# Optimization experiments

Hardware: AMD Instinct MI355X
Metric: run time of the kernel (lower is better)

## Reference

```python
import jax, jax.numpy as jnp
import numpy as np

D = 896      # mm_hidden_size
H = 8        # num heads
HD = D // H  # head dim = 112
M = 8        # num_memory_tokens
P = 196      # patch_size
EPS = 1e-12


def _layernorm(x, g, b):
    mu = jnp.mean(x, axis=-1, keepdims=True)
    var = jnp.mean(jnp.square(x - mu), axis=-1, keepdims=True)
    return (x - mu) * jax.lax.rsqrt(var + EPS) * g + b


def setup_inputs() -> dict:
    key = jax.random.key(0)
    ks = jax.random.split(key, 12)
    F = 32
    s = 0.02
    return {
        "image_features": jax.random.normal(ks[0], (F, P, D), jnp.float32),
        "initial_memory": jax.random.normal(ks[1], (M, P, D), jnp.float32),
        "qW": jax.random.normal(ks[2], (D, D), jnp.float32) * s,
        "qb": jnp.zeros((D,), jnp.float32),
        "kW": jax.random.normal(ks[3], (D, D), jnp.float32) * s,
        "kb": jnp.zeros((D,), jnp.float32),
        "vW": jax.random.normal(ks[4], (D, D), jnp.float32) * s,
        "vb": jnp.zeros((D,), jnp.float32),
        "oW": jax.random.normal(ks[5], (D, D), jnp.float32) * s,
        "ob": jnp.zeros((D,), jnp.float32),
        "ln1_g": jnp.ones((D,), jnp.float32),
        "ln1_b": jnp.zeros((D,), jnp.float32),
        "mW": jax.random.normal(ks[6], (D, 4 * D), jnp.float32) * s,
        "mb": jnp.zeros((4 * D,), jnp.float32),
        "pW": jax.random.normal(ks[7], (4 * D, D), jnp.float32) * s,
        "pb": jnp.zeros((D,), jnp.float32),
        "ln2_g": jnp.ones((D,), jnp.float32),
        "ln2_b": jnp.zeros((D,), jnp.float32),
    }


def reference(image_features, initial_memory, qW, qb, kW, kb, vW, vb,
              oW, ob, ln1_g, ln1_b, mW, mb, pW, pb, ln2_g, ln2_b):
    F = image_features.shape[0]
    Lq = M * P            # 1568 query tokens
    Lk = F * P            # kv tokens
    mem = initial_memory.reshape(1, Lq, D)      # [1, Lq, D]
    img = image_features.reshape(1, Lk, D)      # [1, Lk, D]

    def heads(x, L):
        return x.reshape(1, L, H, HD).transpose(0, 2, 1, 3)  # [1,H,L,hd]

    q = heads(mem @ qW + qb, Lq)
    k = heads(img @ kW + kb, Lk)
    v = heads(img @ vW + vb, Lk)

    scores = jnp.einsum('bhqd,bhkd->bhqk', q, k) / np.sqrt(HD).astype(jnp.float32)
    probs = jax.nn.softmax(scores, axis=-1)                  # [1,H,Lq,Lk]
    ctx = jnp.einsum('bhqk,bhkd->bhqd', probs, v)
    ctx = ctx.transpose(0, 2, 1, 3).reshape(1, Lq, D)

    # residual + layernorm epilogue of Attention
    attn_out = _layernorm(ctx @ oW + ob + mem, ln1_g, ln1_b)

    # MLP -> residual + layernorm
    hidden = jax.nn.relu(attn_out @ mW + mb)                 # [1, Lq, 4D]
    out = _layernorm(hidden @ pW + pb + attn_out, ln2_g, ln2_b)

    # frame attention scores: sum over heads and query tokens, avg per frame
    attn_sum = probs.sum(axis=(1, 2))[0]                     # [Lk]
    frame_scores = attn_sum.reshape(F, P).mean(axis=1)       # [F]

    final_memory = out.reshape(M, P, D)
    return final_memory, frame_scores
```

## Files before the change

kernel.cpp:

```cpp
#include <hip/hip_runtime.h>
#include <hip/hip_bf16.h>
#include <math.h>

#define TP_D   896
#define TP_H   8
#define TP_HD  112
#define TP_LQ  1568
#define TP_LK  6272
#define TP_D4  3584
#define TP_F   32
#define TP_P   196

typedef unsigned short u16;
typedef float f32x4 __attribute__((ext_vector_type(4)));
typedef __bf16 bf16x8 __attribute__((ext_vector_type(8)));

__device__ inline float bf2f(u16 u) {
    return __uint_as_float(((unsigned int)u) << 16);
}
__device__ inline u16 f2bf(float f) {
    unsigned int x = __float_as_uint(f);
    unsigned int lsb = (x >> 16) & 1u;
    x += 0x7fffu + lsb;
    return (u16)(x >> 16);
}
__device__ inline ushort4 pack4(float a, float b, float c, float d) {
    return make_ushort4(f2bf(a), f2bf(b), f2bf(c), f2bf(d));
}
__device__ inline int pidx(int row, int col) {
    return row * 128 + (col ^ ((row & 7) << 3));
}

__global__ void cast_f32_bf16(const float* __restrict__ src, u16* __restrict__ dst, int n) {
    int i = (blockIdx.x * blockDim.x + threadIdx.x) * 4;
    if (i + 3 < n) {
        float4 v = *(const float4*)(src + i);
        *(ushort4*)(dst + i) = pack4(v.x, v.y, v.z, v.w);
    } else {
        for (; i < n; ++i) dst[i] = f2bf(src[i]);
    }
}

__global__ void cast_div_bf16(const float* __restrict__ src, const float* __restrict__ l,
                              u16* __restrict__ dst) {
    int i = (blockIdx.x * 256 + threadIdx.x) * 4;
    if (i >= TP_LQ * TP_D) return;
    int q = i / TP_D;
    int col = i - q * TP_D;
    int h = col / TP_HD;
    float inv = 1.f / l[h * TP_LQ + q];
    float4 v = *(const float4*)(src + i);
    *(ushort4*)(dst + i) = pack4(v.x * inv, v.y * inv, v.z * inv, v.w * inv);
}

__global__ void transpose_cast(const float* __restrict__ src, u16* __restrict__ dst, int R, int C) {
    __shared__ float t[32][33];
    int bx = blockIdx.x * 32;
    int by = blockIdx.y * 32;
    int tx = threadIdx.x, ty = threadIdx.y;
#pragma unroll
    for (int j = 0; j < 4; ++j)
        t[ty + j * 8][tx] = src[(size_t)(by + ty + j * 8) * C + bx + tx];
    __syncthreads();
#pragma unroll
    for (int j = 0; j < 4; ++j)
        dst[(size_t)(bx + ty + j * 8) * R + by + tx] = f2bf(t[tx][ty + j * 8]);
}

struct GemmParams {
    const u16* A;  long long aZ; int lda;
    const u16* Bt; long long bZ; int ldb;
    int M, N, K;
    const float* bias;
    float* outF;
    u16* outB; long long cZ; int ldc;
    float scale;
    int hbase;
    int relu;
    int kc;
};

#define LDS_STRIDE 56

template <int MODE>
__global__ __launch_bounds__(256, 2) void gemm_bf16(GemmParams p) {
    __shared__ u16 lsA[128 * LDS_STRIDE];
    __shared__ u16 lsB[128 * LDS_STRIDE];

    const int tid = threadIdx.x;
    const int z = blockIdx.z;
    const u16* A;
    const u16* Bt;
    if (MODE == 6) {
        A  = p.A  + (size_t)z * p.kc;
        Bt = p.Bt + (size_t)z * p.kc;
    } else {
        A  = p.A  + (size_t)z * p.aZ;
        Bt = p.Bt + (size_t)z * p.bZ;
    }
    const int m0 = blockIdx.y * 128;
    const int n0 = blockIdx.x * 128;

    const int lane = tid & 63;
    const int w = tid >> 6;
    const int wm = (w >> 1) * 64, wn = (w & 1) * 64;
    const int c = lane & 15, q = lane >> 4;

    f32x4 acc[4][4];
#pragma unroll
    for (int i = 0; i < 4; ++i)
#pragma unroll
        for (int j = 0; j < 4; ++j) acc[i][j] = 0.f;

    const int r0 = tid >> 2;
    const int c8 = (tid & 3) * 8;
    int arow0 = m0 + r0;      if (arow0 >= p.M) arow0 = p.M - 1;
    int arow1 = m0 + r0 + 64; if (arow1 >= p.M) arow1 = p.M - 1;
    int brow0 = n0 + r0;      if (brow0 >= p.N) brow0 = p.N - 1;
    int brow1 = n0 + r0 + 64; if (brow1 >= p.N) brow1 = p.N - 1;
    const u16* a0 = A  + (size_t)arow0 * p.lda + c8;
    const u16* a1 = A  + (size_t)arow1 * p.lda + c8;
    const u16* b0 = Bt + (size_t)brow0 * p.ldb + c8;
    const u16* b1 = Bt + (size_t)brow1 * p.ldb + c8;

    const int KT = (p.K + 31) >> 5;
    for (int kt = 0; kt < KT; ++kt) {
        const int k0 = kt << 5;
        const bool valid = (k0 + c8 + 8) <= p.K;
        uint4 zv = make_uint4(0, 0, 0, 0);
        uint4 va0 = valid ? *(const uint4*)(a0 + k0) : zv;
        uint4 va1 = valid ? *(const uint4*)(a1 + k0) : zv;
        uint4 vb0 = valid ? *(const uint4*)(b0 + k0) : zv;
        uint4 vb1 = valid ? *(const uint4*)(b1 + k0) : zv;
        *(uint4*)(&lsA[r0 * LDS_STRIDE + c8])        = va0;
        *(uint4*)(&lsA[(r0 + 64) * LDS_STRIDE + c8]) = va1;
        *(uint4*)(&lsB[r0 * LDS_STRIDE + c8])        = vb0;
        *(uint4*)(&lsB[(r0 + 64) * LDS_STRIDE + c8]) = vb1;
        __syncthreads();

        bf16x8 af[4], bfv[4];
#pragma unroll
        for (int mi = 0; mi < 4; ++mi)
            af[mi] = *(const bf16x8*)(&lsA[(wm + mi * 16 + c) * LDS_STRIDE + q * 8]);
#pragma unroll
        for (int ni = 0; ni < 4; ++ni)
            bfv[ni] = *(const bf16x8*)(&lsB[(wn + ni * 16 + c) * LDS_STRIDE + q * 8]);
#pragma unroll
        for (int mi = 0; mi < 4; ++mi)
#pragma unroll
            for (int ni = 0; ni < 4; ++ni)
                acc[mi][ni] = __builtin_amdgcn_mfma_f32_16x16x32_bf16(af[mi], bfv[ni], acc[mi][ni], 0, 0, 0);
        __syncthreads();
    }

    if (MODE == 7) {
#pragma unroll
        for (int ni = 0; ni < 4; ++ni) {
            const int col = n0 + wn + ni * 16 + c;
            const float bv = p.bias[col];
#pragma unroll
            for (int mi = 0; mi < 4; ++mi) {
                const int mbase = m0 + wm + mi * 16 + q * 4;
                f32x4 a = acc[mi][ni];
                *(ushort4*)(p.outB + (size_t)col * p.ldc + mbase) =
                    pack4(a[0] + bv, a[1] + bv, a[2] + bv, a[3] + bv);
            }
        }
        return;
    }

#pragma unroll
    for (int mi = 0; mi < 4; ++mi) {
#pragma unroll
        for (int r = 0; r < 4; ++r) {
            const int row = m0 + wm + mi * 16 + q * 4 + r;
            if (row >= p.M) continue;
#pragma unroll
            for (int ni = 0; ni < 4; ++ni) {
                const int col = n0 + wn + ni * 16 + c;
                float v = acc[mi][ni][r];
                if (MODE == 4) {
                    v += p.bias[col];
                    if (p.relu) v = v > 0.f ? v : 0.f;
                    p.outB[(size_t)row * p.ldc + col] = f2bf(v);
                } else if (MODE == 6) {
                    atomicAdd(&p.outF[(size_t)row * p.ldc + col], v);
                }
            }
        }
    }
}

__global__ __launch_bounds__(256, 2) void attn_fused(
        const u16* __restrict__ Qf, const u16* __restrict__ Kf,
        const u16* __restrict__ Vtf, u16* __restrict__ E,
        float* __restrict__ lsum, float* __restrict__ ctxF, float scale) {
    __shared__ u16 lsQ[128 * 128];
    __shared__ u16 lsB[128 * 40];
    __shared__ u16 lsP[128 * 128];

    const int ks  = blockIdx.x;
    const int m0  = blockIdx.y * 128;
    const int h   = blockIdx.z;
    const int tid = threadIdx.x;
    const int lane = tid & 63, w = tid >> 6;
    const int wm = (w >> 1) * 64, wn = (w & 1) * 64;
    const int c = lane & 15, q = lane >> 4;

    {
        const int row = tid >> 1;
        const int half = (tid & 1) * 64;
        int qrow = m0 + row; if (qrow > TP_LQ - 1) qrow = TP_LQ - 1;
        const u16* src = Qf + (size_t)qrow * TP_D + h * TP_HD;
#pragma unroll
        for (int j = 0; j < 8; ++j) {
            int col = half + j * 8;
            uint4 v = make_uint4(0, 0, 0, 0);
            if (col + 8 <= TP_HD) v = *(const uint4*)(src + col);
            *(uint4*)(&lsQ[pidx(row, col)]) = v;
        }
    }

    const int r0 = tid >> 2;
    const int c8 = (tid & 3) * 8;
    const int keybase = ks * 896;

    f32x4 acc_pv[4][4];
#pragma unroll
    for (int i = 0; i < 4; ++i)
#pragma unroll
        for (int j = 0; j < 4; ++j) acc_pv[i][j] = 0.f;
    float rs[4] = {0.f, 0.f, 0.f, 0.f};

    for (int kb = 0; kb < 7; ++kb) {
        const int kblk = keybase + kb * 128;
        f32x4 acc_s[4][4];
#pragma unroll
        for (int i = 0; i < 4; ++i)
#pragma unroll
            for (int j = 0; j < 4; ++j) acc_s[i][j] = 0.f;

#pragma unroll
        for (int kt = 0; kt < 4; ++kt) {
            const int k0 = kt * 32;
            const bool valid = (k0 + c8 + 8) <= TP_HD;
            uint4 zv = make_uint4(0, 0, 0, 0);
            uint4 vb0 = valid ? *(const uint4*)(Kf + (size_t)(kblk + r0) * TP_D + h * TP_HD + k0 + c8) : zv;
            uint4 vb1 = valid ? *(const uint4*)(Kf + (size_t)(kblk + r0 + 64) * TP_D + h * TP_HD + k0 + c8) : zv;
            __syncthreads();
            *(uint4*)(&lsB[r0 * 40 + c8])        = vb0;
            *(uint4*)(&lsB[(r0 + 64) * 40 + c8]) = vb1;
            __syncthreads();
            bf16x8 af[4], bfv[4];
#pragma unroll
            for (int mi = 0; mi < 4; ++mi)
                af[mi] = *(const bf16x8*)(&lsQ[pidx(wm + mi * 16 + c, k0 + q * 8)]);
#pragma unroll
            for (int ni = 0; ni < 4; ++ni)
                bfv[ni] = *(const bf16x8*)(&lsB[(wn + ni * 16 + c) * 40 + q * 8]);
#pragma unroll
            for (int mi = 0; mi < 4; ++mi)
#pragma unroll
                for (int ni = 0; ni < 4; ++ni)
                    acc_s[mi][ni] = __builtin_amdgcn_mfma_f32_16x16x32_bf16(bfv[ni], af[mi], acc_s[mi][ni], 0, 0, 0);
        }

        __syncthreads();
#pragma unroll
        for (int mi = 0; mi < 4; ++mi) {
            const int prow = wm + mi * 16 + c;
            const int qr = m0 + prow;
            const bool qv = qr < TP_LQ;
            float rp = 0.f;
#pragma unroll
            for (int ni = 0; ni < 4; ++ni) {
                float e0, e1, e2, e3;
                {
                    f32x4 a = acc_s[mi][ni];
                    e0 = __expf(fminf(a[0] * scale, 30.f));
                    e1 = __expf(fminf(a[1] * scale, 30.f));
                    e2 = __expf(fminf(a[2] * scale, 30.f));
                    e3 = __expf(fminf(a[3] * scale, 30.f));
                }
                rp += (e0 + e1) + (e2 + e3);
                ushort4 pk = pack4(e0, e1, e2, e3);
                const int kcol = wn + ni * 16 + q * 4;
                if (qv)
                    *(ushort4*)(E + ((size_t)h * TP_LQ + qr) * TP_LK + kblk + kcol) = pk;
                *(ushort4*)(&lsP[pidx(prow, kcol)]) = pk;
            }
            rs[mi] += rp;
        }

#pragma unroll
        for (int kt = 0; kt < 4; ++kt) {
            const int kk = kblk + kt * 32 + c8;
            int d0 = r0;
            int d1 = r0 + 64; if (d1 > TP_HD - 1) d1 = TP_HD - 1;
            uint4 vb0 = *(const uint4*)(Vtf + ((size_t)h * TP_HD + d0) * TP_LK + kk);
            uint4 vb1 = *(const uint4*)(Vtf + ((size_t)h * TP_HD + d1) * TP_LK + kk);
            __syncthreads();
            *(uint4*)(&lsB[r0 * 40 + c8])        = vb0;
            *(uint4*)(&lsB[(r0 + 64) * 40 + c8]) = vb1;
            __syncthreads();
            bf16x8 ap[4], bv[4];
#pragma unroll
            for (int mi = 0; mi < 4; ++mi)
                ap[mi] = *(const bf16x8*)(&lsP[pidx(wm + mi * 16 + c, kt * 32 + q * 8)]);
#pragma unroll
            for (int ni = 0; ni < 4; ++ni)
                bv[ni] = *(const bf16x8*)(&lsB[(wn + ni * 16 + c) * 40 + q * 8]);
#pragma unroll
            for (int mi = 0; mi < 4; ++mi)
#pragma unroll
                for (int ni = 0; ni < 4; ++ni)
                    acc_pv[mi][ni] = __builtin_amdgcn_mfma_f32_16x16x32_bf16(ap[mi], bv[ni], acc_pv[mi][ni], 0, 0, 0);
        }
    }

#pragma unroll
    for (int mi = 0; mi < 4; ++mi) {
        float rp = rs[mi];
        rp += __shfl_xor(rp, 16, 64);
        rp += __shfl_xor(rp, 32, 64);
        const int qr = m0 + wm + mi * 16 + c;
        if (q == 0 && qr < TP_LQ) atomicAdd(&lsum[h * TP_LQ + qr], rp);
    }
#pragma unroll
    for (int mi = 0; mi < 4; ++mi) {
#pragma unroll
        for (int r = 0; r < 4; ++r) {
            const int qr = m0 + wm + mi * 16 + q * 4 + r;
            if (qr >= TP_LQ) continue;
#pragma unroll
            for (int ni = 0; ni < 4; ++ni) {
                const int d = wn + ni * 16 + c;
                if (d < TP_HD)
                    atomicAdd(&ctxF[(size_t)qr * TP_D + h * TP_HD + d], acc_pv[mi][ni][r]);
            }
        }
    }
}

__global__ void colsum_kernel(const u16* __restrict__ E, const float* __restrict__ l,
                              float* __restrict__ colsum, int nrows) {
    int c4 = blockIdx.x * 256 + threadIdx.x;
    if (c4 >= TP_LK / 4) return;
    int chunk = (nrows + gridDim.y - 1) / gridDim.y;
    int r0 = blockIdx.y * chunk;
    int r1 = r0 + chunk; if (r1 > nrows) r1 = nrows;
    float a0 = 0.f, a1 = 0.f, a2 = 0.f, a3 = 0.f;
    for (int r = r0; r < r1; ++r) {
        float inv = 1.f / l[r];
        ushort4 u = ((const ushort4*)(E + (size_t)r * TP_LK))[c4];
        a0 += bf2f(u.x) * inv; a1 += bf2f(u.y) * inv;
        a2 += bf2f(u.z) * inv; a3 += bf2f(u.w) * inv;
    }
    atomicAdd(&colsum[4 * c4 + 0], a0);
    atomicAdd(&colsum[4 * c4 + 1], a1);
    atomicAdd(&colsum[4 * c4 + 2], a2);
    atomicAdd(&colsum[4 * c4 + 3], a3);
}

__global__ __launch_bounds__(256) void layernorm_rows(const float* __restrict__ x,
        const float* __restrict__ bias, const float* __restrict__ res,
        const float* __restrict__ g, const float* __restrict__ b,
        float* __restrict__ outF, u16* __restrict__ outB) {
    const int tid = threadIdx.x;
    const float* xr = x + (size_t)blockIdx.x * TP_D;
    const float* rr = res + (size_t)blockIdx.x * TP_D;
    float v[4];
#pragma unroll
    for (int i = 0; i < 4; ++i) {
        int idx = tid + i * 256;
        v[i] = (idx < TP_D) ? (xr[idx] + bias[idx] + rr[idx]) : 0.f;
    }
    float s = v[0] + v[1] + v[2] + v[3];
    __shared__ float red[4];
#pragma unroll
    for (int o = 32; o > 0; o >>= 1) s += __shfl_xor(s, o, 64);
    if ((tid & 63) == 0) red[tid >> 6] = s;
    __syncthreads();
    const float mu = (red[0] + red[1] + red[2] + red[3]) * (1.f / TP_D);
    __syncthreads();
    float ss = 0.f;
#pragma unroll
    for (int i = 0; i < 4; ++i) {
        int idx = tid + i * 256;
        if (idx < TP_D) { float d = v[i] - mu; ss += d * d; }
    }
#pragma unroll
    for (int o = 32; o > 0; o >>= 1) ss += __shfl_xor(ss, o, 64);
    if ((tid & 63) == 0) red[tid >> 6] = ss;
    __syncthreads();
    const float var = (red[0] + red[1] + red[2] + red[3]) * (1.f / TP_D);
    const float rs = rsqrtf(var + 1e-12f);
    float* of = outF + (size_t)blockIdx.x * TP_D;
    u16* obp = outB ? outB + (size_t)blockIdx.x * TP_D : nullptr;
#pragma unroll
    for (int i = 0; i < 4; ++i) {
        int idx = tid + i * 256;
        if (idx < TP_D) {
            float y = (v[i] - mu) * rs * g[idx] + b[idx];
            of[idx] = y;
            if (obp) obp[idx] = f2bf(y);
        }
    }
}

__global__ void frame_scores_kernel(const float* __restrict__ colsum, float* __restrict__ out) {
    const int tid = threadIdx.x;
    float v = (tid < TP_P) ? colsum[blockIdx.x * TP_P + tid] : 0.f;
    __shared__ float red[4];
#pragma unroll
    for (int o = 32; o > 0; o >>= 1) v += __shfl_xor(v, o, 64);
    if ((tid & 63) == 0) red[tid >> 6] = v;
    __syncthreads();
    if (tid == 0) out[blockIdx.x] = (red[0] + red[1] + red[2] + red[3]) * (1.f / TP_P);
}

extern "C" void kernel_launch(void* const* d_in, const int* in_sizes, int n_in,
                              void* d_out, int out_size, void* d_ws, size_t ws_size,
                              hipStream_t stream) {
    const float* img  = (const float*)d_in[0];
    const float* mem  = (const float*)d_in[1];
    const float* qW   = (const float*)d_in[2];
    const float* qb   = (const float*)d_in[3];
    const float* kW   = (const float*)d_in[4];
    const float* kb   = (const float*)d_in[5];
    const float* vW   = (const float*)d_in[6];
    const float* vb   = (const float*)d_in[7];
    const float* oW   = (const float*)d_in[8];
    const float* ob   = (const float*)d_in[9];
    const float* ln1g = (const float*)d_in[10];
    const float* ln1b = (const float*)d_in[11];
    const float* mW   = (const float*)d_in[12];
    const float* mb   = (const float*)d_in[13];
    const float* pW   = (const float*)d_in[14];
    const float* pb   = (const float*)d_in[15];
    const float* ln2g = (const float*)d_in[16];
    const float* ln2b = (const float*)d_in[17];
    float* out = (float*)d_out;

    char* base = (char*)d_ws;
    size_t off = 0;
    auto take = [&](size_t nbytes) -> void* {
        void* p = base + off;
        off += (nbytes + 255) & ~(size_t)255;
        return p;
    };

    u16* imgB  = (u16*)take((size_t)TP_LK * TP_D * 2);
    u16* memB  = (u16*)take((size_t)TP_LQ * TP_D * 2);
    u16* qWt   = (u16*)take((size_t)TP_D * TP_D * 2);
    u16* kWt   = (u16*)take((size_t)TP_D * TP_D * 2);
    u16* vWt   = (u16*)take((size_t)TP_D * TP_D * 2);
    u16* oWt   = (u16*)take((size_t)TP_D * TP_D * 2);
    u16* mWt   = (u16*)take((size_t)TP_D * TP_D4 * 2);
    u16* pWt   = (u16*)take((size_t)TP_D * TP_D4 * 2);
    u16* Qf    = (u16*)take((size_t)TP_LQ * TP_D * 2);
    u16* Kf    = (u16*)take((size_t)TP_LK * TP_D * 2);
    u16* Vtf   = (u16*)take((size_t)TP_LK * TP_D * 2);
    float* ctxF  = (float*)take((size_t)TP_LQ * TP_D * 4);
    u16* ctxB  = (u16*)take((size_t)TP_LQ * TP_D * 2);
    float* pre1  = (float*)take((size_t)TP_LQ * TP_D * 4);
    float* attn  = (float*)take((size_t)TP_LQ * TP_D * 4);
    u16* attnB = (u16*)take((size_t)TP_LQ * TP_D * 2);
    u16* hidden= (u16*)take((size_t)TP_LQ * TP_D4 * 2);
    float* pre2  = (float*)take((size_t)TP_LQ * TP_D * 4);
    float* colsum= (float*)take((size_t)TP_LK * 4);
    float* lsum  = (float*)take((size_t)TP_H * TP_LQ * 4);
    u16* E     = (u16*)take((size_t)TP_H * TP_LQ * TP_LK * 2);

    cast_f32_bf16<<<(TP_LK * TP_D / 4 + 255) / 256, 256, 0, stream>>>(img, imgB, TP_LK * TP_D);
    cast_f32_bf16<<<(TP_LQ * TP_D / 4 + 255) / 256, 256, 0, stream>>>(mem, memB, TP_LQ * TP_D);
    transpose_cast<<<dim3(28, 28), dim3(32, 8), 0, stream>>>(qW, qWt, TP_D, TP_D);
    transpose_cast<<<dim3(28, 28), dim3(32, 8), 0, stream>>>(kW, kWt, TP_D, TP_D);
    transpose_cast<<<dim3(28, 28), dim3(32, 8), 0, stream>>>(vW, vWt, TP_D, TP_D);
    transpose_cast<<<dim3(28, 28), dim3(32, 8), 0, stream>>>(oW, oWt, TP_D, TP_D);
    transpose_cast<<<dim3(TP_D4 / 32, TP_D / 32), dim3(32, 8), 0, stream>>>(mW, mWt, TP_D, TP_D4);
    transpose_cast<<<dim3(TP_D / 32, TP_D4 / 32), dim3(32, 8), 0, stream>>>(pW, pWt, TP_D4, TP_D);
    hipMemsetAsync(colsum, 0, (size_t)TP_LK * 4, stream);
    hipMemsetAsync(lsum, 0, (size_t)TP_H * TP_LQ * 4, stream);
    hipMemsetAsync(ctxF, 0, (size_t)TP_LQ * TP_D * 4, stream);
    hipMemsetAsync(pre1, 0, (size_t)TP_LQ * TP_D * 4, stream);
    hipMemsetAsync(pre2, 0, (size_t)TP_LQ * TP_D * 4, stream);

    {
        GemmParams p{};
        p.A = memB; p.aZ = 0; p.lda = TP_D;
        p.Bt = qWt; p.bZ = 0; p.ldb = TP_D;
        p.M = TP_LQ; p.N = TP_D; p.K = TP_D;
        p.bias = qb; p.outB = Qf; p.ldc = TP_D; p.relu = 0;
        gemm_bf16<4><<<dim3(7, 13, 1), 256, 0, stream>>>(p);
    }
    {
        GemmParams p{};
        p.A = imgB; p.aZ = 0; p.lda = TP_D;
        p.Bt = kWt; p.bZ = 0; p.ldb = TP_D;
        p.M = TP_LK; p.N = TP_D; p.K = TP_D;
        p.bias = kb; p.outB = Kf; p.ldc = TP_D; p.relu = 0;
        gemm_bf16<4><<<dim3(7, 49, 1), 256, 0, stream>>>(p);
    }
    {
        GemmParams p{};
        p.A = imgB; p.aZ = 0; p.lda = TP_D;
        p.Bt = vWt; p.bZ = 0; p.ldb = TP_D;
        p.M = TP_LK; p.N = TP_D; p.K = TP_D;
        p.bias = vb; p.outB = Vtf; p.ldc = TP_LK;
        gemm_bf16<7><<<dim3(7, 49, 1), 256, 0, stream>>>(p);
    }

    const float scale = 0.09449111825230679f;
    attn_fused<<<dim3(7, 13, TP_H), 256, 0, stream>>>(Qf, Kf, Vtf, E, lsum, ctxF, scale);
    colsum_kernel<<<dim3(7, 224), 256, 0, stream>>>(E, lsum, colsum, TP_H * TP_LQ);
    cast_div_bf16<<<(TP_LQ * TP_D / 4 + 255) / 256, 256, 0, stream>>>(ctxF, lsum, ctxB);

    {
        GemmParams p{};
        p.A = ctxB; p.lda = TP_D;
        p.Bt = oWt; p.ldb = TP_D;
        p.M = TP_LQ; p.N = TP_D; p.K = 448; p.kc = 448;
        p.outF = pre1; p.ldc = TP_D;
        gemm_bf16<6><<<dim3(7, 13, 2), 256, 0, stream>>>(p);
    }
    layernorm_rows<<<TP_LQ, 256, 0, stream>>>(pre1, ob, mem, ln1g, ln1b, attn, attnB);

    {
        GemmParams p{};
        p.A = attnB; p.aZ = 0; p.lda = TP_D;
        p.Bt = mWt; p.bZ = 0; p.ldb = TP_D;
        p.M = TP_LQ; p.N = TP_D4; p.K = TP_D;
        p.bias = mb; p.outB = hidden; p.ldc = TP_D4; p.relu = 1;
        gemm_bf16<4><<<dim3(28, 13, 1), 256, 0, stream>>>(p);
    }
    {
        GemmParams p{};
        p.A = hidden; p.lda = TP_D4;
        p.Bt = pWt; p.ldb = TP_D4;
        p.M = TP_LQ; p.N = TP_D; p.K = 896; p.kc = 896;
        p.outF = pre2; p.ldc = TP_D;
        gemm_bf16<6><<<dim3(7, 13, 4), 256, 0, stream>>>(p);
    }
    layernorm_rows<<<TP_LQ, 256, 0, stream>>>(pre2, pb, attn, ln2g, ln2b, out, nullptr);

    frame_scores_kernel<<<TP_F, 256, 0, stream>>>(colsum, out + (size_t)TP_LQ * TP_D);
}
```

Measured before the change: 557.9 us.

## Halve GEMM N-tile to 64, raise occupancy, merge casts and memsets

The bf16 GEMM becomes templated on its N-tile width, and every GEMM launch now uses a 128x64 tile with twice as many blocks and launch bounds allowing 4 blocks per CU. This targets better CU fill and latency hiding for GEMMs whose grids were small relative to the CU count, at the cost of less B-operand reuse per block. The two input casts are merged into one kernel, and the five zero-fill memsets become one contiguous memset over reordered buffers, cutting launch overhead.

```diff
diff --git a/kernel.cpp b/kernel.cpp
--- a/kernel.cpp
+++ b/kernel.cpp
@@ -31,14 +31,14 @@
     return row * 128 + (col ^ ((row & 7) << 3));
 }
 
-__global__ void cast_f32_bf16(const float* __restrict__ src, u16* __restrict__ dst, int n) {
+__global__ void cast2_f32_bf16(const float* __restrict__ src0, u16* __restrict__ dst0, int n0,
+                               const float* __restrict__ src1, u16* __restrict__ dst1, int n1) {
     int i = (blockIdx.x * blockDim.x + threadIdx.x) * 4;
-    if (i + 3 < n) {
-        float4 v = *(const float4*)(src + i);
-        *(ushort4*)(dst + i) = pack4(v.x, v.y, v.z, v.w);
-    } else {
-        for (; i < n; ++i) dst[i] = f2bf(src[i]);
-    }
+    const float* s; u16* d; int n;
+    if (i < n0) { s = src0; d = dst0; n = n0; }
+    else        { i -= n0; s = src1; d = dst1; n = n1; if (i >= n) return; }
+    float4 v = *(const float4*)(s + i);
+    *(ushort4*)(d + i) = pack4(v.x, v.y, v.z, v.w);
 }
 
 __global__ void cast_div_bf16(const float* __restrict__ src, const float* __restrict__ l,
@@ -68,49 +68,44 @@
 }
 
 struct GemmParams {
-    const u16* A;  long long aZ; int lda;
-    const u16* Bt; long long bZ; int ldb;
+    const u16* A;  int lda;
+    const u16* Bt; int ldb;
     int M, N, K;
     const float* bias;
     float* outF;
-    u16* outB; long long cZ; int ldc;
-    float scale;
-    int hbase;
+    u16* outB; int ldc;
     int relu;
     int kc;
 };
 
 #define LDS_STRIDE 56
 
-template <int MODE>
-__global__ __launch_bounds__(256, 2) void gemm_bf16(GemmParams p) {
+template <int MODE, int NT>
+__global__ __launch_bounds__(256, 4) void gemm_bf16(GemmParams p) {
     __shared__ u16 lsA[128 * LDS_STRIDE];
-    __shared__ u16 lsB[128 * LDS_STRIDE];
+    __shared__ u16 lsB[NT * 32 * LDS_STRIDE];
 
     const int tid = threadIdx.x;
     const int z = blockIdx.z;
-    const u16* A;
-    const u16* Bt;
+    const u16* A  = p.A;
+    const u16* Bt = p.Bt;
     if (MODE == 6) {
-        A  = p.A  + (size_t)z * p.kc;
-        Bt = p.Bt + (size_t)z * p.kc;
-    } else {
-        A  = p.A  + (size_t)z * p.aZ;
-        Bt = p.Bt + (size_t)z * p.bZ;
+        A  += (size_t)z * p.kc;
+        Bt += (size_t)z * p.kc;
     }
     const int m0 = blockIdx.y * 128;
-    const int n0 = blockIdx.x * 128;
+    const int n0 = blockIdx.x * (NT * 32);
 
     const int lane = tid & 63;
     const int w = tid >> 6;
-    const int wm = (w >> 1) * 64, wn = (w & 1) * 64;
+    const int wm = (w >> 1) * 64, wn = (w & 1) * (16 * NT);
     const int c = lane & 15, q = lane >> 4;
 
-    f32x4 acc[4][4];
+    f32x4 acc[4][NT];
 #pragma unroll
     for (int i = 0; i < 4; ++i)
 #pragma unroll
-        for (int j = 0; j < 4; ++j) acc[i][j] = 0.f;
+        for (int j = 0; j < NT; ++j) acc[i][j] = 0.f;
 
     const int r0 = tid >> 2;
     const int c8 = (tid & 3) * 8;
@@ -131,31 +126,32 @@
         uint4 va0 = valid ? *(const uint4*)(a0 + k0) : zv;
         uint4 va1 = valid ? *(const uint4*)(a1 + k0) : zv;
         uint4 vb0 = valid ? *(const uint4*)(b0 + k0) : zv;
-        uint4 vb1 = valid ? *(const uint4*)(b1 + k0) : zv;
+        uint4 vb1 = (NT == 4 && valid) ? *(const uint4*)(b1 + k0) : zv;
         *(uint4*)(&lsA[r0 * LDS_STRIDE + c8])        = va0;
         *(uint4*)(&lsA[(r0 + 64) * LDS_STRIDE + c8]) = va1;
         *(uint4*)(&lsB[r0 * LDS_STRIDE + c8])        = vb0;
-        *(uint4*)(&lsB[(r0 + 64) * LDS_STRIDE + c8]) = vb1;
+        if (NT == 4)
+            *(uint4*)(&lsB[(r0 + 64) * LDS_STRIDE + c8]) = vb1;
         __syncthreads();
 
-        bf16x8 af[4], bfv[4];
+        bf16x8 af[4], bfv[NT];
 #pragma unroll
         for (int mi = 0; mi < 4; ++mi)
             af[mi] = *(const bf16x8*)(&lsA[(wm + mi * 16 + c) * LDS_STRIDE + q * 8]);
 #pragma unroll
-        for (int ni = 0; ni < 4; ++ni)
+        for (int ni = 0; ni < NT; ++ni)
             bfv[ni] = *(const bf16x8*)(&lsB[(wn + ni * 16 + c) * LDS_STRIDE + q * 8]);
 #pragma unroll
         for (int mi = 0; mi < 4; ++mi)
 #pragma unroll
-            for (int ni = 0; ni < 4; ++ni)
+            for (int ni = 0; ni < NT; ++ni)
                 acc[mi][ni] = __builtin_amdgcn_mfma_f32_16x16x32_bf16(af[mi], bfv[ni], acc[mi][ni], 0, 0, 0);
         __syncthreads();
     }
 
     if (MODE == 7) {
 #pragma unroll
-        for (int ni = 0; ni < 4; ++ni) {
+        for (int ni = 0; ni < NT; ++ni) {
             const int col = n0 + wn + ni * 16 + c;
             const float bv = p.bias[col];
 #pragma unroll
@@ -176,7 +172,7 @@
             const int row = m0 + wm + mi * 16 + q * 4 + r;
             if (row >= p.M) continue;
 #pragma unroll
-            for (int ni = 0; ni < 4; ++ni) {
+            for (int ni = 0; ni < NT; ++ni) {
                 const int col = n0 + wn + ni * 16 + c;
                 float v = acc[mi][ni][r];
                 if (MODE == 4) {
@@ -394,14 +390,14 @@
     if ((tid & 63) == 0) red[tid >> 6] = ss;
     __syncthreads();
     const float var = (red[0] + red[1] + red[2] + red[3]) * (1.f / TP_D);
-    const float rs = rsqrtf(var + 1e-12f);
+    const float rsq = rsqrtf(var + 1e-12f);
     float* of = outF + (size_t)blockIdx.x * TP_D;
     u16* obp = outB ? outB + (size_t)blockIdx.x * TP_D : nullptr;
 #pragma unroll
     for (int i = 0; i < 4; ++i) {
         int idx = tid + i * 256;
         if (idx < TP_D) {
-            float y = (v[i] - mu) * rs * g[idx] + b[idx];
+            float y = (v[i] - mu) * rsq * g[idx] + b[idx];
             of[idx] = y;
             if (obp) obp[idx] = f2bf(y);
         }
@@ -461,54 +457,53 @@
     u16* Qf    = (u16*)take((size_t)TP_LQ * TP_D * 2);
     u16* Kf    = (u16*)take((size_t)TP_LK * TP_D * 2);
     u16* Vtf   = (u16*)take((size_t)TP_LK * TP_D * 2);
-    float* ctxF  = (float*)take((size_t)TP_LQ * TP_D * 4);
     u16* ctxB  = (u16*)take((size_t)TP_LQ * TP_D * 2);
-    float* pre1  = (float*)take((size_t)TP_LQ * TP_D * 4);
     float* attn  = (float*)take((size_t)TP_LQ * TP_D * 4);
     u16* attnB = (u16*)take((size_t)TP_LQ * TP_D * 2);
     u16* hidden= (u16*)take((size_t)TP_LQ * TP_D4 * 2);
+    u16* E     = (u16*)take((size_t)TP_H * TP_LQ * TP_LK * 2);
+    float* ctxF  = (float*)take((size_t)TP_LQ * TP_D * 4);
+    float* pre1  = (float*)take((size_t)TP_LQ * TP_D * 4);
     float* pre2  = (float*)take((size_t)TP_LQ * TP_D * 4);
     float* colsum= (float*)take((size_t)TP_LK * 4);
     float* lsum  = (float*)take((size_t)TP_H * TP_LQ * 4);
-    u16* E     = (u16*)take((size_t)TP_H * TP_LQ * TP_LK * 2);
-
-    cast_f32_bf16<<<(TP_LK * TP_D / 4 + 255) / 256, 256, 0, stream>>>(img, imgB, TP_LK * TP_D);
-    cast_f32_bf16<<<(TP_LQ * TP_D / 4 + 255) / 256, 256, 0, stream>>>(mem, memB, TP_LQ * TP_D);
+    size_t zlen = (char*)(lsum + TP_H * TP_LQ) - (char*)ctxF;
+
+    {
+        int n0 = TP_LK * TP_D, n1 = TP_LQ * TP_D;
+        cast2_f32_bf16<<<((n0 + n1) / 4 + 255) / 256, 256, 0, stream>>>(img, imgB, n0, mem, memB, n1);
+    }
     transpose_cast<<<dim3(28, 28), dim3(32, 8), 0, stream>>>(qW, qWt, TP_D, TP_D);
     transpose_cast<<<dim3(28, 28), dim3(32, 8), 0, stream>>>(kW, kWt, TP_D, TP_D);
     transpose_cast<<<dim3(28, 28), dim3(32, 8), 0, stream>>>(vW, vWt, TP_D, TP_D);
     transpose_cast<<<dim3(28, 28), dim3(32, 8), 0, stream>>>(oW, oWt, TP_D, TP_D);
     transpose_cast<<<dim3(TP_D4 / 32, TP_D / 32), dim3(32, 8), 0, stream>>>(mW, mWt, TP_D, TP_D4);
     transpose_cast<<<dim3(TP_D / 32, TP_D4 / 32), dim3(32, 8), 0, stream>>>(pW, pWt, TP_D4, TP_D);
-    hipMemsetAsync(colsum, 0, (size_t)TP_LK * 4, stream);
-    hipMemsetAsync(lsum, 0, (size_t)TP_H * TP_LQ * 4, stream);
-    hipMemsetAsync(ctxF, 0, (size_t)TP_LQ * TP_D * 4, stream);
-    hipMemsetAsync(pre1, 0, (size_t)TP_LQ * TP_D * 4, stream);
-    hipMemsetAsync(pre2, 0, (size_t)TP_LQ * TP_D * 4, stream);
+    hipMemsetAsync(ctxF, 0, zlen, stream);
 
     {
         GemmParams p{};
-        p.A = memB; p.aZ = 0; p.lda = TP_D;
-        p.Bt = qWt; p.bZ = 0; p.ldb = TP_D;
+        p.A = memB; p.lda = TP_D;
+        p.Bt = qWt; p.ldb = TP_D;
         p.M = TP_LQ; p.N = TP_D; p.K = TP_D;
         p.bias = qb; p.outB = Qf; p.ldc = TP_D; p.relu = 0;
-        gemm_bf16<4><<<dim3(7, 13, 1), 256, 0, stream>>>(p);
+        gemm_bf16<4, 2><<<dim3(14, 13, 1), 256, 0, stream>>>(p);
     }
     {
         GemmParams p{};
-        p.A = imgB; p.aZ = 0; p.lda = TP_D;
-        p.Bt = kWt; p.bZ = 0; p.ldb = TP_D;
+        p.A = imgB; p.lda = TP_D;
+        p.Bt = kWt; p.ldb = TP_D;
         p.M = TP_LK; p.N = TP_D; p.K = TP_D;
         p.bias = kb; p.outB = Kf; p.ldc = TP_D; p.relu = 0;
-        gemm_bf16<4><<<dim3(7, 49, 1), 256, 0, stream>>>(p);
+        gemm_bf16<4, 2><<<dim3(14, 49, 1), 256, 0, stream>>>(p);
     }
     {
         GemmParams p{};
-        p.A = imgB; p.aZ = 0; p.lda = TP_D;
-        p.Bt = vWt; p.bZ = 0; p.ldb = TP_D;
+        p.A = imgB; p.lda = TP_D;
+        p.Bt = vWt; p.ldb = TP_D;
         p.M = TP_LK; p.N = TP_D; p.K = TP_D;
         p.bias = vb; p.outB = Vtf; p.ldc = TP_LK;
-        gemm_bf16<7><<<dim3(7, 49, 1), 256, 0, stream>>>(p);
+        gemm_bf16<7, 2><<<dim3(14, 49, 1), 256, 0, stream>>>(p);
     }
 
     const float scale = 0.09449111825230679f;
@@ -522,17 +517,17 @@
         p.Bt = oWt; p.ldb = TP_D;
         p.M = TP_LQ; p.N = TP_D; p.K = 448; p.kc = 448;
         p.outF = pre1; p.ldc = TP_D;
-        gemm_bf16<6><<<dim3(7, 13, 2), 256, 0, stream>>>(p);
+        gemm_bf16<6, 2><<<dim3(14, 13, 2), 256, 0, stream>>>(p);
     }
     layernorm_rows<<<TP_LQ, 256, 0, stream>>>(pre1, ob, mem, ln1g, ln1b, attn, attnB);
 
     {
         GemmParams p{};
-        p.A = attnB; p.aZ = 0; p.lda = TP_D;
-        p.Bt = mWt; p.bZ = 0; p.ldb = TP_D;
+        p.A = attnB; p.lda = TP_D;
+        p.Bt = mWt; p.ldb = TP_D;
         p.M = TP_LQ; p.N = TP_D4; p.K = TP_D;
         p.bias = mb; p.outB = hidden; p.ldc = TP_D4; p.relu = 1;
-        gemm_bf16<4><<<dim3(28, 13, 1), 256, 0, stream>>>(p);
+        gemm_bf16<4, 2><<<dim3(56, 13, 1), 256, 0, stream>>>(p);
     }
     {
         GemmParams p{};
@@ -540,7 +535,7 @@
         p.Bt = pWt; p.ldb = TP_D4;
         p.M = TP_LQ; p.N = TP_D; p.K = 896; p.kc = 896;
         p.outF = pre2; p.ldc = TP_D;
-        gemm_bf16<6><<<dim3(7, 13, 4), 256, 0, stream>>>(p);
+        gemm_bf16<6, 2><<<dim3(14, 13, 4), 256, 0, stream>>>(p);
     }
     layernorm_rows<<<TP_LQ, 256, 0, stream>>>(pre2, pb, attn, ln2g, ln2b, out, nullptr);
 
```

New measurement: 543.6 us. 2.6% less time.
